# Performance work log

Hardware: AMD Instinct MI355X
Metric: run time of the kernel (lower is better)

Reference implementation:

```python
import jax, jax.numpy as jnp
import numpy as np

B, S, D_IN = 4, 4096, 4096
G, R, GROUP_DIM = 8, 256, 512  # num_groups, rank per group, out_features // num_groups


def setup_inputs() -> dict:
    key = jax.random.key(0)
    k1, k2, k3 = jax.random.split(key, 3)
    scale = 1.0 / np.sqrt(D_IN)
    hidden_states = jax.random.normal(k1, (B, S, D_IN), dtype=jnp.float32)
    VT_w = jax.random.normal(k2, (G * R, D_IN), dtype=jnp.float32) * scale  # nn.Linear weight layout (out, in)
    U_w = jax.random.normal(k3, (G, GROUP_DIM, R), dtype=jnp.float32) * (1.0 / np.sqrt(R))  # per-group Linear weights
    return {"hidden_states": hidden_states, "VT_w": VT_w, "U_w": U_w}


def reference(hidden_states, VT_w, U_w):
    # shared low-rank down-projection: (B,S,D_in) @ VT_w.T -> (B,S,G*R)
    latent = jnp.einsum('bsd,rd->bsr', hidden_states, VT_w)
    # since all ranks are equal, the per-group loop + concat is a block-diagonal GEMM:
    latent = latent.reshape(B, S, G, R)
    out = jnp.einsum('bsgr,gor->bsgo', latent, U_w)  # per-group up-projection (o = group_dim)
    return out.reshape(B, S, G * GROUP_DIM)
```

## Files before the change

kernel.cpp:

```cpp
#include <hip/hip_runtime.h>
#include <stdint.h>


typedef short  bf16x8  __attribute__((ext_vector_type(8)));
typedef float  f32x4   __attribute__((ext_vector_type(4)));
typedef ushort ushort8 __attribute__((ext_vector_type(8)));
typedef float  flt4    __attribute__((ext_vector_type(4)));

__device__ __forceinline__ void gload_lds16(const ushort* g, ushort* l) {
    __builtin_amdgcn_global_load_lds(
        (const __attribute__((address_space(1))) uint32_t*)g,
        (__attribute__((address_space(3))) uint32_t*)l, 16, 0, 0);
}

__device__ __forceinline__ ushort f2bf(float f) {
    union { float f; uint32_t u; } c; c.f = f;
    uint32_t u = c.u;
    uint32_t r = (u + 0x7FFFu + ((u >> 16) & 1u)) >> 16;
    return (ushort)r;
}

__device__ __forceinline__ uint32_t cvtpk(float lo, float hi) {
    uint32_t r;
    asm("v_cvt_pk_bf16_f32 %0, %1, %2" : "=v"(r) : "v"(lo), "v"(hi));
    return r;
}

__device__ __forceinline__ void conv_seg(const float* __restrict__ in,
                                         ushort* __restrict__ out,
                                         long n8, int bid, int nblk) {
    const long stride = (long)nblk * 256;
    for (long i = (long)bid * 256 + threadIdx.x; i < n8; i += stride) {
        flt4 a = ((const flt4*)in)[2 * i];
        flt4 b = ((const flt4*)in)[2 * i + 1];
        ushort8 o;
        o[0] = f2bf(a[0]); o[1] = f2bf(a[1]); o[2] = f2bf(a[2]); o[3] = f2bf(a[3]);
        o[4] = f2bf(b[0]); o[5] = f2bf(b[1]); o[6] = f2bf(b[2]); o[7] = f2bf(b[3]);
        ((ushort8*)out)[i] = o;
    }
}

__global__ __launch_bounds__(256) void convert_vt_u_kernel(
    const float* __restrict__ vt_f, ushort* __restrict__ vt_b, long nVT8,
    const float* __restrict__ u_f,  ushort* __restrict__ u_b,  long nU8)
{
    const int b = blockIdx.x;
    if (b < 896) conv_seg(vt_f, vt_b, nVT8, b,       896);
    else         conv_seg(u_f,  u_b,  nU8,  b - 896, 128);
}

__device__ __forceinline__ void store_out(ushort* p, float v) { *p = f2bf(v); }
__device__ __forceinline__ void store_out(float*  p, float v) { *p = v; }

__global__ __launch_bounds__(256) void gemm1_fused_kernel(
    const float* __restrict__ Af,
    const ushort* __restrict__ B,
    ushort* __restrict__ C,
    int lda, int ldb, int ldc, int K, int bxShift)
{
    __shared__ ushort As[128 * 64];
    __shared__ ushort Bs[2][128 * 64];

    const int tid  = threadIdx.x;
    const int lane = tid & 63;
    const int wave = tid >> 6;

    const int bid = blockIdx.x;
    const int xcd = bid & 7;
    const int rr  = bid >> 3;
    const int by  = xcd * 16 + (rr >> bxShift);
    const int bx  = rr & ((1 << bxShift) - 1);

    const int row0 = by * 128;
    const int col0 = bx * 128;

    const int wr = wave >> 1;
    const int wc = wave & 1;

    const int l15    = lane & 15;
    const int lq     = lane >> 4;
    const int lrow   = lane >> 3;
    const int lchunk = lane & 7;
    const int l7     = lane & 7;

    f32x4 acc[4][4] = {};
    flt4 pa[8];

    const float*  aF   = Af + (size_t)(row0 + wave * 32 + lrow) * lda + lchunk * 8;
    const ushort* bPtr = B  + (size_t)(col0 + wave * 32 + lrow) * ldb
                            + ((lchunk ^ lrow) * 8);
    ushort* aDstBase = As + wave * 4 * 512 + lrow * 64 + ((lchunk ^ lrow) * 8);

    const int nkt = K / 64;

    #pragma unroll
    for (int i = 0; i < 4; ++i) {
        const float* src = aF + (size_t)(i * 8) * lda;
        pa[2 * i]     = *(const flt4*)(src);
        pa[2 * i + 1] = *(const flt4*)(src + 4);
    }
    #pragma unroll
    for (int i = 0; i < 4; ++i)
        gload_lds16(bPtr + (size_t)i * 8 * ldb, Bs[0] + (wave * 4 + i) * 512);

    for (int kt = 0; kt < nkt; ++kt) {
        __syncthreads();

        #pragma unroll
        for (int i = 0; i < 4; ++i) {
            uint4 w;
            w.x = cvtpk(pa[2*i][0],   pa[2*i][1]);
            w.y = cvtpk(pa[2*i][2],   pa[2*i][3]);
            w.z = cvtpk(pa[2*i+1][0], pa[2*i+1][1]);
            w.w = cvtpk(pa[2*i+1][2], pa[2*i+1][3]);
            *(uint4*)(aDstBase + i * 512) = w;
        }
        __syncthreads();

        if (kt + 1 < nkt) {
            const int kN = (kt + 1) * 64;
            #pragma unroll
            for (int i = 0; i < 4; ++i)
                gload_lds16(bPtr + (size_t)i * 8 * ldb + kN,
                            Bs[(kt + 1) & 1] + (wave * 4 + i) * 512);
            #pragma unroll
            for (int i = 0; i < 4; ++i) {
                const float* src = aF + (size_t)(i * 8) * lda + kN;
                pa[2 * i]     = *(const flt4*)(src);
                pa[2 * i + 1] = *(const flt4*)(src + 4);
            }
        }

        const ushort* bCur = Bs[kt & 1];
        #pragma unroll
        for (int kk = 0; kk < 2; ++kk) {
            const int rc = ((((kk << 2) | lq) ^ l7) << 3);
            bf16x8 af[4], bfr[4];
            #pragma unroll
            for (int m = 0; m < 4; ++m)
                af[m] = *(const bf16x8*)&As[(wr * 64 + m * 16 + l15) * 64 + rc];
            #pragma unroll
            for (int n = 0; n < 4; ++n)
                bfr[n] = *(const bf16x8*)&bCur[(wc * 64 + n * 16 + l15) * 64 + rc];
            #pragma unroll
            for (int m = 0; m < 4; ++m)
                #pragma unroll
                for (int n = 0; n < 4; ++n)
                    acc[m][n] = __builtin_amdgcn_mfma_f32_16x16x32_bf16(
                        af[m], bfr[n], acc[m][n], 0, 0, 0);
        }
    }

    #pragma unroll
    for (int m = 0; m < 4; ++m) {
        #pragma unroll
        for (int r = 0; r < 4; ++r) {
            const size_t row = (size_t)(row0 + wr * 64 + m * 16 + lq * 4 + r);
            ushort* cRow = C + row * ldc + col0 + wc * 64 + l15;
            #pragma unroll
            for (int n = 0; n < 4; ++n)
                cRow[n * 16] = f2bf(acc[m][n][r]);
        }
    }
}

template <typename TOUT>
__global__ __launch_bounds__(512) void gemm_bt8_kernel(
    const ushort* __restrict__ A,
    const ushort* __restrict__ B,
    TOUT* __restrict__ C,
    int lda, int ldb, int ldc, int K, int bxShift,
    long aOffZ, long bOffZ, long cOffZ)
{
    A += (size_t)blockIdx.z * aOffZ;
    B += (size_t)blockIdx.z * bOffZ;
    C += (size_t)blockIdx.z * cOffZ;

    __shared__ ushort As[128 * 64];
    __shared__ ushort Bs[128 * 64];

    const int tid  = threadIdx.x;
    const int lane = tid & 63;
    const int wave = tid >> 6;

    const int bid = blockIdx.x;
    const int xcd = bid & 7;
    const int rr  = bid >> 3;
    const int by  = xcd * 16 + (rr >> bxShift);
    const int bx  = rr & ((1 << bxShift) - 1);

    const int row0 = by * 128;
    const int col0 = bx * 128;

    const int wr = wave >> 2;
    const int wc = wave & 3;

    const int l15    = lane & 15;
    const int lq     = lane >> 4;
    const int lrow   = lane >> 3;
    const int lchunk = lane & 7;

    f32x4 acc[4][2] = {};

    const ushort* aPtr = A + (size_t)(row0 + wave * 8 + lrow) * lda + lchunk * 8;
    const ushort* bPtr = B + (size_t)(col0 + wave * 8 + lrow) * ldb + lchunk * 8;
    const int ldsseg = wave * 512;

    const int nkt = K / 64;
    for (int kt = 0; kt < nkt; ++kt) {
        const int kOff = kt * 64;
        __syncthreads();
        #pragma unroll
        for (int i = 0; i < 2; ++i) {
            gload_lds16(aPtr + (size_t)i * 64 * lda + kOff, As + i * 4096 + ldsseg);
            gload_lds16(bPtr + (size_t)i * 64 * ldb + kOff, Bs + i * 4096 + ldsseg);
        }
        __syncthreads();

        #pragma unroll
        for (int kk = 0; kk < 2; ++kk) {
            bf16x8 af[4], bfr[2];
            #pragma unroll
            for (int m = 0; m < 4; ++m)
                af[m] = *(const bf16x8*)&As[(wr * 64 + m * 16 + l15) * 64 + kk * 32 + lq * 8];
            #pragma unroll
            for (int n = 0; n < 2; ++n)
                bfr[n] = *(const bf16x8*)&Bs[(wc * 32 + n * 16 + l15) * 64 + kk * 32 + lq * 8];
            #pragma unroll
            for (int m = 0; m < 4; ++m)
                #pragma unroll
                for (int n = 0; n < 2; ++n)
                    acc[m][n] = __builtin_amdgcn_mfma_f32_16x16x32_bf16(
                        af[m], bfr[n], acc[m][n], 0, 0, 0);
        }
    }

    #pragma unroll
    for (int m = 0; m < 4; ++m) {
        #pragma unroll
        for (int r = 0; r < 4; ++r) {
            const size_t row = (size_t)(row0 + wr * 64 + m * 16 + lq * 4 + r);
            TOUT* cRow = C + row * ldc + col0 + wc * 32 + l15;
            #pragma unroll
            for (int n = 0; n < 2; ++n)
                store_out(cRow + n * 16, acc[m][n][r]);
        }
    }
}

extern "C" void kernel_launch(void* const* d_in, const int* in_sizes, int n_in,
                              void* d_out, int out_size, void* d_ws, size_t ws_size,
                              hipStream_t stream) {
    const float* hidden_f = (const float*)d_in[0];
    const float* VT_f     = (const float*)d_in[1];
    const float* U_f      = (const float*)d_in[2];
    float* out = (float*)d_out;

    const long nVT  = 2048L * 4096L;
    const long nU   = 8L * 512L * 256L;
    const long nLat = 16384L * 2048L;

    ushort *vt_b, *u_b, *lat_b;
    const size_t needA = (size_t)(nVT + nU + nLat) * 2;
    ushort* w = (ushort*)d_ws;
    lat_b = w;  u_b = lat_b + nLat;
    if (ws_size >= needA) vt_b = u_b + nU;
    else                  vt_b = (ushort*)d_out;

    convert_vt_u_kernel<<<dim3(1024), dim3(256), 0, stream>>>(
        VT_f, vt_b, nVT / 8, U_f, u_b, nU / 8);

    gemm1_fused_kernel<<<dim3(2048, 1, 1), dim3(256), 0, stream>>>(
        hidden_f, vt_b, lat_b, 4096, 4096, 2048, 4096, 4);

    gemm_bt8_kernel<float><<<dim3(512, 1, 8), dim3(512), 0, stream>>>(
        lat_b, u_b, out, 2048, 256, 4096, 256, 2,
        256L, 512L * 256L, 512L);
}
```

Before: 476.6 us.

## Deepen fp32 A prefetch in GEMM1 and XOR-swizzle LDS in second GEMM

GEMM1 now keeps two register banks of fp32 A tiles, prefetching two k-steps ahead. It replaces __syncthreads with explicit s_waitcnt/s_barrier so the B global->LDS load for the next tile overlaps the current compute. The second GEMM applies the same XOR chunk swizzle to LDS addresses as GEMM1, which is meant to remove bank conflicts on the MFMA fragment reads. The change costs more registers, and the hand-written vmcnt counts must match the real number of in-flight loads or the kernel becomes wrong.

Result: slower. 515.7 us (+8.2%).

```diff
diff --git a/kernel.cpp b/kernel.cpp
--- a/kernel.cpp
+++ b/kernel.cpp
@@ -52,6 +52,63 @@
 __device__ __forceinline__ void store_out(ushort* p, float v) { *p = f2bf(v); }
 __device__ __forceinline__ void store_out(float*  p, float v) { *p = v; }
 
+
+#define G1_BODY(BANK, KT, ISSB, ISSA, WB) do { \
+     \
+    asm volatile("s_waitcnt lgkmcnt(0)" ::: "memory"); \
+    __builtin_amdgcn_s_barrier(); \
+     \
+    _Pragma("unroll") \
+    for (int i = 0; i < 4; ++i) { \
+        uint4 w_; \
+        w_.x = cvtpk(BANK[2*i][0],   BANK[2*i][1]); \
+        w_.y = cvtpk(BANK[2*i][2],   BANK[2*i][3]); \
+        w_.z = cvtpk(BANK[2*i+1][0], BANK[2*i+1][1]); \
+        w_.w = cvtpk(BANK[2*i+1][2], BANK[2*i+1][3]); \
+        *(uint4*)(aDstBase + i * 512) = w_; \
+    } \
+     \
+    if (ISSB) { \
+        _Pragma("unroll") \
+        for (int i = 0; i < 4; ++i) \
+            gload_lds16(bPtr + (size_t)i * 8 * ldb + ((KT) + 1) * 64, \
+                        Bs[((KT) + 1) & 1] + (wave * 4 + i) * 512); \
+    } \
+     \
+    asm volatile("s_waitcnt vmcnt(" #WB ") lgkmcnt(0)" ::: "memory"); \
+    __builtin_amdgcn_s_barrier(); \
+     \
+    if (ISSA) { \
+        _Pragma("unroll") \
+        for (int i = 0; i < 4; ++i) { \
+            const float* s_ = aF + (size_t)(i * 8) * lda + ((KT) + 2) * 64; \
+            BANK[2*i]   = *(const flt4*)(s_); \
+            BANK[2*i+1] = *(const flt4*)(s_ + 4); \
+        } \
+    } \
+     \
+    { \
+        const ushort* bCur = Bs[(KT) & 1]; \
+        _Pragma("unroll") \
+        for (int kk = 0; kk < 2; ++kk) { \
+            const int rc = ((((kk << 2) | lq) ^ l7) << 3); \
+            bf16x8 af[4], bfr[4]; \
+            _Pragma("unroll") \
+            for (int m = 0; m < 4; ++m) \
+                af[m] = *(const bf16x8*)&As[(wr * 64 + m * 16 + l15) * 64 + rc]; \
+            _Pragma("unroll") \
+            for (int n = 0; n < 4; ++n) \
+                bfr[n] = *(const bf16x8*)&bCur[(wc * 64 + n * 16 + l15) * 64 + rc]; \
+            _Pragma("unroll") \
+            for (int m = 0; m < 4; ++m) \
+                _Pragma("unroll") \
+                for (int n = 0; n < 4; ++n) \
+                    acc[m][n] = __builtin_amdgcn_mfma_f32_16x16x32_bf16( \
+                        af[m], bfr[n], acc[m][n], 0, 0, 0); \
+        } \
+    } \
+} while (0)
+
 __global__ __launch_bounds__(256) void gemm1_fused_kernel(
     const float* __restrict__ Af,
     const ushort* __restrict__ B,
@@ -84,7 +141,7 @@
     const int l7     = lane & 7;
 
     f32x4 acc[4][4] = {};
-    flt4 pa[8];
+    flt4 pa[8], pb[8];
 
     const float*  aF   = Af + (size_t)(row0 + wave * 32 + lrow) * lda + lchunk * 8;
     const ushort* bPtr = B  + (size_t)(col0 + wave * 32 + lrow) * ldb
@@ -95,60 +152,26 @@
 
     #pragma unroll
     for (int i = 0; i < 4; ++i) {
-        const float* src = aF + (size_t)(i * 8) * lda;
-        pa[2 * i]     = *(const flt4*)(src);
-        pa[2 * i + 1] = *(const flt4*)(src + 4);
+        const float* s = aF + (size_t)(i * 8) * lda;
+        pa[2*i] = *(const flt4*)(s);  pa[2*i+1] = *(const flt4*)(s + 4);
     }
     #pragma unroll
     for (int i = 0; i < 4; ++i)
         gload_lds16(bPtr + (size_t)i * 8 * ldb, Bs[0] + (wave * 4 + i) * 512);
-
-    for (int kt = 0; kt < nkt; ++kt) {
-        __syncthreads();
-
-        #pragma unroll
-        for (int i = 0; i < 4; ++i) {
-            uint4 w;
-            w.x = cvtpk(pa[2*i][0],   pa[2*i][1]);
-            w.y = cvtpk(pa[2*i][2],   pa[2*i][3]);
-            w.z = cvtpk(pa[2*i+1][0], pa[2*i+1][1]);
-            w.w = cvtpk(pa[2*i+1][2], pa[2*i+1][3]);
-            *(uint4*)(aDstBase + i * 512) = w;
-        }
-        __syncthreads();
-
-        if (kt + 1 < nkt) {
-            const int kN = (kt + 1) * 64;
-            #pragma unroll
-            for (int i = 0; i < 4; ++i)
-                gload_lds16(bPtr + (size_t)i * 8 * ldb + kN,
-                            Bs[(kt + 1) & 1] + (wave * 4 + i) * 512);
-            #pragma unroll
-            for (int i = 0; i < 4; ++i) {
-                const float* src = aF + (size_t)(i * 8) * lda + kN;
-                pa[2 * i]     = *(const flt4*)(src);
-                pa[2 * i + 1] = *(const flt4*)(src + 4);
-            }
-        }
-
-        const ushort* bCur = Bs[kt & 1];
-        #pragma unroll
-        for (int kk = 0; kk < 2; ++kk) {
-            const int rc = ((((kk << 2) | lq) ^ l7) << 3);
-            bf16x8 af[4], bfr[4];
-            #pragma unroll
-            for (int m = 0; m < 4; ++m)
-                af[m] = *(const bf16x8*)&As[(wr * 64 + m * 16 + l15) * 64 + rc];
-            #pragma unroll
-            for (int n = 0; n < 4; ++n)
-                bfr[n] = *(const bf16x8*)&bCur[(wc * 64 + n * 16 + l15) * 64 + rc];
-            #pragma unroll
-            for (int m = 0; m < 4; ++m)
-                #pragma unroll
-                for (int n = 0; n < 4; ++n)
-                    acc[m][n] = __builtin_amdgcn_mfma_f32_16x16x32_bf16(
-                        af[m], bfr[n], acc[m][n], 0, 0, 0);
-        }
+    #pragma unroll
+    for (int i = 0; i < 4; ++i) {
+        const float* s = aF + (size_t)(i * 8) * lda + 64;
+        pb[2*i] = *(const flt4*)(s);  pb[2*i+1] = *(const flt4*)(s + 4);
+    }
+
+    for (int kt = 0; kt + 2 < nkt; kt += 2) {
+        G1_BODY(pa, kt,     1, 1, 12);
+        G1_BODY(pb, kt + 1, 1, 1, 12);
+    }
+    {
+        const int kt = nkt - 2;
+        G1_BODY(pa, kt,     1, 0, 12);
+        G1_BODY(pb, kt + 1, 0, 0, 0);
     }
 
     #pragma unroll
@@ -199,11 +222,14 @@
     const int lq     = lane >> 4;
     const int lrow   = lane >> 3;
     const int lchunk = lane & 7;
+    const int l7     = lane & 7;
 
     f32x4 acc[4][2] = {};
 
-    const ushort* aPtr = A + (size_t)(row0 + wave * 8 + lrow) * lda + lchunk * 8;
-    const ushort* bPtr = B + (size_t)(col0 + wave * 8 + lrow) * ldb + lchunk * 8;
+    const ushort* aPtr = A + (size_t)(row0 + wave * 8 + lrow) * lda
+                           + ((lchunk ^ lrow) * 8);
+    const ushort* bPtr = B + (size_t)(col0 + wave * 8 + lrow) * ldb
+                           + ((lchunk ^ lrow) * 8);
     const int ldsseg = wave * 512;
 
     const int nkt = K / 64;
@@ -219,13 +245,14 @@
 
         #pragma unroll
         for (int kk = 0; kk < 2; ++kk) {
+            const int rc = ((((kk << 2) | lq) ^ l7) << 3);
             bf16x8 af[4], bfr[2];
             #pragma unroll
             for (int m = 0; m < 4; ++m)
-                af[m] = *(const bf16x8*)&As[(wr * 64 + m * 16 + l15) * 64 + kk * 32 + lq * 8];
+                af[m] = *(const bf16x8*)&As[(wr * 64 + m * 16 + l15) * 64 + rc];
             #pragma unroll
             for (int n = 0; n < 2; ++n)
-                bfr[n] = *(const bf16x8*)&Bs[(wc * 32 + n * 16 + l15) * 64 + kk * 32 + lq * 8];
+                bfr[n] = *(const bf16x8*)&Bs[(wc * 32 + n * 16 + l15) * 64 + rc];
             #pragma unroll
             for (int m = 0; m < 4; ++m)
                 #pragma unroll
```
